# Performance work log

Hardware: AMD Instinct MI355X
Metric: run time of the kernel (lower is better)

The kernel has to match this reference:

```python
import jax, jax.numpy as jnp
import numpy as np


def _conv1x1(x, w, b):
    # x: (B,Ci,H,W), w: (Co,Ci) -> (B,Co,H,W)
    return jnp.einsum('bchw,oc->bohw', x, w) + b[None, :, None, None]


def _conv3x3(x, w, b):
    # x: (B,Ci,H,W), w: (Co,Ci,3,3), stride 1, padding 1 ('SAME')
    y = jax.lax.conv_general_dilated(
        x, w, window_strides=(1, 1), padding='SAME',
        dimension_numbers=('NCHW', 'OIHW', 'NCHW'))
    return y + b[None, :, None, None]


def setup_inputs() -> dict:
    key = jax.random.key(0)
    ks = jax.random.split(key, 10)
    N, B, Cc, Cf, H, W = 3, 8, 128, 256, 64, 64
    s = 0.05  # weight scale to keep attention logits well-conditioned
    return {
        'contexts': jax.random.normal(ks[0], (N, B, Cc, 2 * H, 2 * W), jnp.float32),
        'mainstream': jax.random.normal(ks[1], (B, Cf, H, W), jnp.float32),
        'Wc_w': jax.random.normal(ks[2], (Cc, Cc), jnp.float32) * s,
        'Wc_b': jax.random.normal(ks[3], (Cc,), jnp.float32) * s,
        'Wf_w': jax.random.normal(ks[4], (Cc, Cf), jnp.float32) * s,
        'Wf_b': jax.random.normal(ks[5], (Cc,), jnp.float32) * s,
        'Wk_w': jax.random.normal(ks[6], (Cc, Cf), jnp.float32) * s,
        'Wk_b': jax.random.normal(ks[7], (Cc,), jnp.float32) * s,
        'Wv_w': jax.random.normal(ks[8], (Cc, Cf, 3, 3), jnp.float32) * s,
        'Wv_b': jax.random.normal(ks[9], (Cc,), jnp.float32) * s,
    }


def reference(contexts, mainstream, Wc_w, Wc_b, Wf_w, Wf_b, Wk_w, Wk_b, Wv_w, Wv_b):
    N, B, Cc = contexts.shape[0], contexts.shape[1], contexts.shape[2]
    H, W = mainstream.shape[2], mainstream.shape[3]

    q = _conv1x1(mainstream, Wf_w, Wf_b)        # (B,Cc,H,W) queries
    mkey = _conv1x1(mainstream, Wk_w, Wk_b)     # (B,Cc,H,W) mainline keys
    vals = _conv3x3(mainstream, Wv_w, Wv_b)     # (B,Cc,H,W) mainline values
    ckeys = jax.vmap(lambda c: _conv1x1(c, Wc_w, Wc_b))(contexts)  # (N,B,Cc,2H,2W)

    # unfold 2x2 sub-pixel blocks: (.., 2H, 2W) -> (.., H, 2, W, 2)
    ckeys = ckeys.reshape(N, B, Cc, H, 2, W, 2)
    cfeat = contexts.reshape(N, B, Cc, H, 2, W, 2)

    # per-pixel cross-attention logits: context keys . query
    logits_ctx = jnp.einsum('nbchiwj,bchw->nbhiwj', ckeys, q)      # (N,B,H,2,W,2)
    # mainline key . query (same logit for all 4 sub-pixels)
    logit_main = jnp.einsum('bchw,bchw->bhw', mkey, q)[None, :, :, None, :, None]
    logits = jnp.concatenate(
        [logits_ctx, jnp.broadcast_to(logit_main, (1, B, H, 2, W, 2))], axis=0)

    attn = jax.nn.softmax(logits, axis=0)                          # (N+1,B,H,2,W,2)

    vfeat = jnp.broadcast_to(vals[None, :, :, :, None, :, None],
                             (1, B, Cc, H, 2, W, 2))
    feats = jnp.concatenate([cfeat, vfeat], axis=0)                # (N+1,B,Cc,H,2,W,2)

    out = jnp.einsum('nbhiwj,nbchiwj->bchiwj', attn, feats)        # (B,Cc,H,2,W,2)
    return out.reshape(B, Cc, 2 * H, 2 * W)
```

## Files before the change

### kernel.cpp

```cpp
#include <hip/hip_runtime.h>

#define NCTX 3
#define B 8
#define CC 128
#define CF 256
#define H 64
#define W 64
#define HW 4096
#define YX 16384

#define WS_QT    0
#define WS_VALS  4194304
#define WS_BIAS  8388608
#define WS_LM    8421376
#define WS_WALL  8454144
#define WS_MSP   8552960
#define WS_WB    13013504
#define WS_WALLO 13160960

typedef __attribute__((ext_vector_type(8))) short bf16x8;
typedef __attribute__((ext_vector_type(4))) float f32x4;
typedef __attribute__((ext_vector_type(8))) unsigned short u16x8;

__device__ __forceinline__ unsigned short f2b(float f) {
    union { float f; unsigned u; } c; c.f = f;
    unsigned u = c.u + 0x7FFFu + ((c.u >> 16) & 1u);
    return (unsigned short)(u >> 16);
}
__device__ __forceinline__ float b2f(unsigned short u) {
    union { unsigned u; float f; } c; c.u = ((unsigned)u) << 16;
    return c.f;
}

__global__ __launch_bounds__(256) void k0(
    const float* __restrict__ Wc_w, const float* __restrict__ Wc_b,
    const float* __restrict__ Wf_w, const float* __restrict__ Wf_b,
    const float* __restrict__ Wk_w, const float* __restrict__ Wk_b,
    const float* __restrict__ Wv, const float* __restrict__ ms,
    unsigned short* __restrict__ Wall, unsigned short* __restrict__ Wallo,
    float* __restrict__ bias448, unsigned short* __restrict__ Wb,
    unsigned short* __restrict__ msP) {
    __shared__ float Ls[32][65];
    int blk = blockIdx.x;
    int t = threadIdx.x;
    if (blk < 448) {
        int o = blk * 256 + t;
        int ci8 = o & 7;
        int idx = o >> 3;
        int row = idx % 448;
        int sc4 = idx / 448;
        int f = (sc4 >> 2) * 32 + (sc4 & 3) * 8 + ci8;
        float w;
        if (row < 128) {
            float s = 0.f;
            for (int o2 = 0; o2 < 128; ++o2) s += Wc_w[o2 * 128 + row] * Wf_w[o2 * 256 + f];
            w = s;
        } else if (row < 384) {
            int p = (row - 128) >> 1;
            w = (row & 1) ? Wk_w[p * 256 + f] : Wf_w[p * 256 + f];
        } else if (row == 384) {
            float s = 0.f;
            for (int o2 = 0; o2 < 128; ++o2) s += Wc_b[o2] * Wf_w[o2 * 256 + f];
            w = s;
        } else w = 0.f;
        unsigned short hi = f2b(w);
        Wall[o] = hi;
        Wallo[o] = f2b(w - b2f(hi));
        if (o < 448) {
            float bb;
            if (o < 128) {
                float s = 0.f;
                for (int o2 = 0; o2 < 128; ++o2) s += Wc_w[o2 * 128 + o] * Wf_b[o2];
                bb = s;
            } else if (o < 384) {
                int p = (o - 128) >> 1;
                bb = (o & 1) ? Wk_b[p] : Wf_b[p];
            } else if (o == 384) {
                float s = 0.f;
                for (int o2 = 0; o2 < 128; ++o2) s += Wc_b[o2] * Wf_b[o2];
                bb = s;
            } else if (o == 385) bb = -1.f;
            else bb = 0.f;
            bias448[o] = bb;
        }
    } else if (blk < 1600) {
        int o = (blk - 448) * 256 + t;
        int ci8 = o & 7;
        int co  = (o >> 3) & 127;
        int c4  = (o >> 10) & 3;
        int s   = (o >> 12) & 7;
        int khw = o >> 15;
        int ci  = s * 32 + c4 * 8 + ci8;
        int kh  = khw / 3, kw = khw - kh * 3;
        Wb[o] = f2b(Wv[((co * 256 + ci) * 3 + kh) * 3 + kw]);
    } else if (blk < 1860) {
        int i = (blk - 1600) * 256 + t;
        if (i < 66560) {
            size_t off;
            if (i < 33792) {
                int x = i % 66; int r = i / 66;
                int g = r & 31, rowi = (r >> 5) & 1, b = r >> 6;
                off = ((((size_t)b * 66 + rowi * 65) * 32) + g) * 66 + x;
            } else {
                int k = i - 33792;
                int xi = k & 1; int g = (k >> 1) & 31; int y1 = (k >> 6) & 63; int b = k >> 12;
                off = ((((size_t)b * 66 + (y1 + 1)) * 32) + g) * 66 + xi * 65;
            }
            *(u16x8*)&msP[off * 8] = (u16x8){0, 0, 0, 0, 0, 0, 0, 0};
        }
    } else {
        int local = blk - 1860;
        int s = local & 7;
        int h = (local >> 3) & 63;
        int b = local >> 9;
        const float* src = ms + ((size_t)b * 256 + s * 32) * HW + h * 64;
        for (int l = t; l < 2048; l += 256) {
            int ci = l >> 6, w = l & 63;
            Ls[ci][w] = src[ci * HW + w];
        }
        __syncthreads();
        int w = t & 63, gi = t >> 6;
        u16x8 vh;
#pragma unroll
        for (int j = 0; j < 8; ++j) vh[j] = f2b(Ls[gi * 8 + j][w]);
        size_t offH = ((((size_t)b * 66 + (h + 1)) * 32) + (s * 4 + gi)) * 66 + (w + 1);
        *(u16x8*)&msP[offH * 8] = vh;
    }
}

__global__ __launch_bounds__(512, 4) void kmm(
    const float* __restrict__ ms, const unsigned short* __restrict__ msP,
    const unsigned short* __restrict__ Wall, const unsigned short* __restrict__ Wallo,
    const float* __restrict__ bias448, const unsigned short* __restrict__ Wb,
    const float* __restrict__ Wv_b,
    float* __restrict__ qt, float* __restrict__ lm, float* __restrict__ vals) {
    __shared__ unsigned char smem[25856] __attribute__((aligned(16)));
    int t = threadIdx.x;
    int lane = t & 63, wid = t >> 6;
    int c4l = lane >> 4, lrow = lane & 15;
    int blk = blockIdx.x;

    if (blk < 512) {
        auto Bs = (unsigned short (*)[2][4][64][8])smem;
        float* biasS = (float*)(smem + 16384);
        float* lmAcc = (float*)(smem + 16384 + 1792);
        int wm = wid >> 1, wn = wid & 1;
        int b = blk >> 6, h = blk & 63;
        int xs = t & 63, g4 = t >> 6;
        int c4w = g4 >> 1, sub = g4 & 1;
        const float* msb = ms + ((size_t)b * 256 + g4 * 4) * HW + h * 64 + xs;
        for (int i = t; i < 448; i += 512) biasS[i] = bias448[i];
        if (t < 64) lmAcc[t] = 0.f;

        f32x4 acc[7][2];
#pragma unroll
        for (int mf = 0; mf < 7; ++mf)
#pragma unroll
            for (int nf = 0; nf < 2; ++nf) acc[mf][nf] = (f32x4){0.f, 0.f, 0.f, 0.f};

        const bf16x8* Whip = (const bf16x8*)Wall;
        const bf16x8* Wlop = (const bf16x8*)Wallo;

#define CVT_WRITE(bufv, F0, F1, F2, F3) do {                                    \
        unsigned short h0 = f2b(F0), h1 = f2b(F1), h2 = f2b(F2), h3 = f2b(F3);  \
        unsigned short q0 = f2b((F0) - b2f(h0)), q1 = f2b((F1) - b2f(h1));      \
        unsigned short q2 = f2b((F2) - b2f(h2)), q3 = f2b((F3) - b2f(h3));      \
        uint2 hw, lw;                                                           \
        hw.x = (unsigned)h0 | ((unsigned)h1 << 16);                             \
        hw.y = (unsigned)h2 | ((unsigned)h3 << 16);                             \
        lw.x = (unsigned)q0 | ((unsigned)q1 << 16);                             \
        lw.y = (unsigned)q2 | ((unsigned)q3 << 16);                             \
        *(uint2*)&Bs[bufv][0][c4w][xs][sub * 4] = hw;                           \
        *(uint2*)&Bs[bufv][1][c4w][xs][sub * 4] = lw;                           \
    } while (0)

        {
            float f0 = msb[0], f1 = msb[HW], f2 = msb[2 * HW], f3 = msb[3 * HW];
            CVT_WRITE(0, f0, f1, f2, f3);
        }
        __syncthreads();

        for (int s = 0; s < 8; ++s) {
            int cur = s & 1;
            float fn0, fn1, fn2, fn3;
            if (s < 7) {
                const float* p = msb + (size_t)(s + 1) * 32 * HW;
                fn0 = p[0]; fn1 = p[HW]; fn2 = p[2 * HW]; fn3 = p[3 * HW];
            }
            bf16x8 bh[2], bl[2];
#pragma unroll
            for (int nf = 0; nf < 2; ++nf) {
                int x = wn * 32 + nf * 16 + lrow;
                bh[nf] = *(const bf16x8*)&Bs[cur][0][c4l][x][0];
                bl[nf] = *(const bf16x8*)&Bs[cur][1][c4l][x][0];
            }
#pragma unroll
            for (int mf = 0; mf < 7; ++mf) {
                size_t widx = (size_t)(s * 4 + c4l) * 448 + wm * 112 + mf * 16 + lrow;
                bf16x8 ah = Whip[widx];
                bf16x8 al = Wlop[widx];
#pragma unroll
                for (int nf = 0; nf < 2; ++nf) {
                    acc[mf][nf] = __builtin_amdgcn_mfma_f32_16x16x32_bf16(ah, bh[nf], acc[mf][nf], 0, 0, 0);
                    acc[mf][nf] = __builtin_amdgcn_mfma_f32_16x16x32_bf16(ah, bl[nf], acc[mf][nf], 0, 0, 0);
                    acc[mf][nf] = __builtin_amdgcn_mfma_f32_16x16x32_bf16(al, bh[nf], acc[mf][nf], 0, 0, 0);
                }
            }
            if (s < 7) CVT_WRITE(cur ^ 1, fn0, fn1, fn2, fn3);
            __syncthreads();
        }
#undef CVT_WRITE

        int px0 = wn * 32;
        float lmp[2] = {0.f, 0.f};
#pragma unroll
        for (int mf = 0; mf < 7; ++mf) {
            int base = wm * 112 + mf * 16;
            int r0 = base + c4l * 4;
            if (base < 128) {
#pragma unroll
                for (int nf = 0; nf < 2; ++nf) {
                    int x = px0 + nf * 16 + lrow;
                    float* dst = qt + ((size_t)b * 128 + r0) * HW + h * 64 + x;
                    f32x4 v = acc[mf][nf];
#pragma unroll
                    for (int j = 0; j < 4; ++j)
                        dst[(size_t)j * HW] = v[j] + biasS[r0 + j];
                }
            } else {
                float b0 = biasS[r0], b1 = biasS[r0 + 1], b2 = biasS[r0 + 2], b3 = biasS[r0 + 3];
#pragma unroll
                for (int nf = 0; nf < 2; ++nf) {
                    f32x4 v = acc[mf][nf];
                    lmp[nf] += (v[0] + b0) * (v[1] + b1) + (v[2] + b2) * (v[3] + b3);
                }
            }
        }
        if (wm != 0) {
#pragma unroll
            for (int nf = 0; nf < 2; ++nf) {
                lmp[nf] += __shfl_xor(lmp[nf], 16);
                lmp[nf] += __shfl_xor(lmp[nf], 32);
            }
            if (c4l == 0) {
#pragma unroll
                for (int nf = 0; nf < 2; ++nf)
                    atomicAdd(&lmAcc[px0 + nf * 16 + lrow], lmp[nf]);
            }
        }
        __syncthreads();
        if (t < 64) lm[b * HW + h * 64 + t] = lmAcc[t];
    } else {
        auto Bs = (unsigned short (*)[6336])smem;
        float* biasS = (float*)(smem + 25344);
        int local = blk - 512;
        int b = local >> 6;
        int hl = local & 63;
        int h = ((hl & 7) << 3) | (hl >> 3);
        int wm = wid >> 1, wn = wid & 1;
        if (t < 128) biasS[t] = Wv_b[t];

        f32x4 acc[2][2];
#pragma unroll
        for (int mf = 0; mf < 2; ++mf)
#pragma unroll
            for (int nf = 0; nf < 2; ++nf) acc[mf][nf] = (f32x4){0.f, 0.f, 0.f, 0.f};

        const bf16x8* Wbp = (const bf16x8*)Wb;

#define STAGE2(bufv, sv) do {                                                       \
        for (int iter = 0; iter < 2; ++iter) {                                      \
            int q0 = iter * 512 + (wid << 6);                                       \
            int q = q0 + lane;                                                      \
            if (q < 792) {                                                          \
                int rc = q / 66; int x = q - rc * 66;                               \
                int r = rc >> 2, c4 = rc & 3;                                       \
                int y = h + r;                               \
                const unsigned short* gp = msP +                                    \
                    (((((size_t)b * 66 + y) * 32) + ((sv) * 4 + c4)) * 66 + x) * 8; \
                unsigned short* lp = &Bs[bufv][q0 * 8];                             \
                __builtin_amdgcn_global_load_lds(                                   \
                    (const __attribute__((address_space(1))) void*)gp,              \
                    (__attribute__((address_space(3))) void*)lp, 16, 0, 0);         \
            }                                                                       \
        }                                                                           \
    } while (0)

        STAGE2(0, 0);
        __syncthreads();

        for (int s = 0; s < 8; ++s) {
            int cur = s & 1;
            if (s < 7) STAGE2(cur ^ 1, s + 1);
#pragma unroll
            for (int khw = 0; khw < 9; ++khw) {
                int kh = khw / 3, kw = khw - 3 * (khw / 3);
                bf16x8 a[2];
#pragma unroll
                for (int mf = 0; mf < 2; ++mf)
                    a[mf] = Wbp[((khw * 8 + s) * 4 + c4l) * 128 + wm * 32 + mf * 16 + lrow];
                bf16x8 bf[2];
#pragma unroll
                for (int nf = 0; nf < 2; ++nf) {
                    int chunk = (kh * 4 + c4l) * 66 + wn * 32 + nf * 16 + lrow + kw;
                    bf[nf] = *(const bf16x8*)&Bs[cur][chunk * 8];
                }
#pragma unroll
                for (int mf = 0; mf < 2; ++mf)
#pragma unroll
                    for (int nf = 0; nf < 2; ++nf)
                        acc[mf][nf] = __builtin_amdgcn_mfma_f32_16x16x32_bf16(
                            a[mf], bf[nf], acc[mf][nf], 0, 0, 0);
            }
            __syncthreads();
        }
#undef STAGE2

#pragma unroll
        for (int mf = 0; mf < 2; ++mf) {
            int co0 = wm * 32 + mf * 16 + c4l * 4;
#pragma unroll
            for (int nf = 0; nf < 2; ++nf) {
                int x = wn * 32 + nf * 16 + lrow;
                float* dst = vals + (((size_t)b * 128 + co0) * HW) + h * 64 + x;
                f32x4 v = acc[mf][nf];
#pragma unroll
                for (int j = 0; j < 4; ++j)
                    dst[(size_t)j * HW] = v[j] + biasS[co0 + j];
            }
        }
    }
}

__global__ __launch_bounds__(256, 2) void k3(
    const float* __restrict__ ctx, const float* __restrict__ qt,
    const float* __restrict__ vals, const float* __restrict__ lm,
    float* __restrict__ out) {
    __shared__ float part[4][3][64];
    __shared__ float attnS[4][64];
    int t = threadIdx.x;
    int lane = t & 63, wv = t >> 6;
    int xg = t & 15, cq = t >> 4;
    int blk = blockIdx.x;
    int b = blk >> 8, y = (blk >> 1) & 127, xh = blk & 1;
    int h = y >> 1;
    int x0 = xh * 64 + xg * 4;
    int p0 = xh * 32 + xg * 2;

    float2 qv[8], vv[8];
    const float* qbase = qt + ((size_t)b * 128 + cq * 8) * HW + h * 64 + p0;
    const float* vbase = vals + ((size_t)b * 128 + cq * 8) * HW + h * 64 + p0;
#pragma unroll
    for (int j = 0; j < 8; ++j) {
        qv[j] = *(const float2*)&qbase[(size_t)j * HW];
        vv[j] = *(const float2*)&vbase[(size_t)j * HW];
    }
    float4 cx[3][8];
#pragma unroll
    for (int n = 0; n < 3; ++n) {
        const float* cb = ctx + ((size_t)(n * 8 + b) * 128 + cq * 8) * YX + (size_t)y * 128 + x0;
#pragma unroll
        for (int j = 0; j < 8; ++j) cx[n][j] = *(const float4*)&cb[(size_t)j * YX];
    }
    float lp[3][4];
#pragma unroll
    for (int n = 0; n < 3; ++n) {
#pragma unroll
        for (int xl = 0; xl < 4; ++xl) lp[n][xl] = 0.f;
#pragma unroll
        for (int j = 0; j < 8; ++j) {
            lp[n][0] += cx[n][j].x * qv[j].x;
            lp[n][1] += cx[n][j].y * qv[j].x;
            lp[n][2] += cx[n][j].z * qv[j].y;
            lp[n][3] += cx[n][j].w * qv[j].y;
        }
    }
#pragma unroll
    for (int n = 0; n < 3; ++n)
#pragma unroll
        for (int xl = 0; xl < 4; ++xl) {
            float v = lp[n][xl];
            v += __shfl_xor(v, 16);
            v += __shfl_xor(v, 32);
            lp[n][xl] = v;
        }
    if (lane < 16) {
#pragma unroll
        for (int n = 0; n < 3; ++n)
#pragma unroll
            for (int xl = 0; xl < 4; ++xl)
                part[wv][n][lane * 4 + xl] = lp[n][xl];
    }
    __syncthreads();
    if (t < 64) {
        float l0 = part[0][0][t] + part[1][0][t] + part[2][0][t] + part[3][0][t];
        float l1 = part[0][1][t] + part[1][1][t] + part[2][1][t] + part[3][1][t];
        float l2 = part[0][2][t] + part[1][2][t] + part[2][2][t] + part[3][2][t];
        float l3 = lm[(size_t)b * HW + h * 64 + xh * 32 + (t >> 1)];
        float m = fmaxf(fmaxf(l0, l1), fmaxf(l2, l3));
        float e0 = __expf(l0 - m), e1 = __expf(l1 - m), e2 = __expf(l2 - m), e3 = __expf(l3 - m);
        float inv = 1.f / (e0 + e1 + e2 + e3);
        attnS[0][t] = e0 * inv; attnS[1][t] = e1 * inv;
        attnS[2][t] = e2 * inv; attnS[3][t] = e3 * inv;
    }
    __syncthreads();
    float a0[4], a1[4], a2[4], a3[4];
#pragma unroll
    for (int xl = 0; xl < 4; ++xl) {
        a0[xl] = attnS[0][xg * 4 + xl];
        a1[xl] = attnS[1][xg * 4 + xl];
        a2[xl] = attnS[2][xg * 4 + xl];
        a3[xl] = attnS[3][xg * 4 + xl];
    }
    float* obase = out + ((size_t)b * 128 + cq * 8) * YX + (size_t)y * 128 + x0;
#pragma unroll
    for (int j = 0; j < 8; ++j) {
        float4 o;
        o.x = a3[0] * vv[j].x + a0[0] * cx[0][j].x + a1[0] * cx[1][j].x + a2[0] * cx[2][j].x;
        o.y = a3[1] * vv[j].x + a0[1] * cx[0][j].y + a1[1] * cx[1][j].y + a2[1] * cx[2][j].y;
        o.z = a3[2] * vv[j].y + a0[2] * cx[0][j].z + a1[2] * cx[1][j].z + a2[2] * cx[2][j].z;
        o.w = a3[3] * vv[j].y + a0[3] * cx[0][j].w + a1[3] * cx[1][j].w + a2[3] * cx[2][j].w;
        *(float4*)&obase[(size_t)j * YX] = o;
    }
}

extern "C" void kernel_launch(void* const* d_in, const int* in_sizes, int n_in,
                              void* d_out, int out_size, void* d_ws, size_t ws_size,
                              hipStream_t stream) {
    const float* ctx  = (const float*)d_in[0];
    const float* ms   = (const float*)d_in[1];
    const float* Wc_w = (const float*)d_in[2];
    const float* Wc_b = (const float*)d_in[3];
    const float* Wf_w = (const float*)d_in[4];
    const float* Wf_b = (const float*)d_in[5];
    const float* Wk_w = (const float*)d_in[6];
    const float* Wk_b = (const float*)d_in[7];
    const float* Wv_w = (const float*)d_in[8];
    const float* Wv_b = (const float*)d_in[9];
    float* out = (float*)d_out;
    float* ws = (float*)d_ws;
    float* qt      = ws + WS_QT;
    float* vals    = ws + WS_VALS;
    float* bias448 = ws + WS_BIAS;
    float* lmp     = ws + WS_LM;
    unsigned short* Wallp  = (unsigned short*)(ws + WS_WALL);
    unsigned short* Wallop = (unsigned short*)(ws + WS_WALLO);
    unsigned short* msPp   = (unsigned short*)(ws + WS_MSP);
    unsigned short* Wbp    = (unsigned short*)(ws + WS_WB);

    hipLaunchKernelGGL(k0, dim3(5956), dim3(256), 0, stream, Wc_w, Wc_b, Wf_w, Wf_b,
                       Wk_w, Wk_b, Wv_w, ms, Wallp, Wallop, bias448, Wbp, msPp);
    hipLaunchKernelGGL(kmm, dim3(1024), dim3(512), 0, stream, ms, msPp, Wallp, Wallop,
                       bias448, Wbp, Wv_b, qt, lmp, vals);
    hipLaunchKernelGGL(k3, dim3(2048), dim3(256), 0, stream, ctx, qt, vals, lmp, out);
}
```

Before: 146.3 us.

## Store q and vals intermediates as bf16, remap k3 blocks, raise occupancy

The matmul kernel now writes the query projection and 3x3 value intermediates in bf16 rather than fp32, halving their write and reread traffic between kmm and k3. k3 unpacks bf16 pairs, defers the value load until after the softmax, restructures the logit reduction per context to cut register pressure, raises its launch bound to 4 blocks per SM, and swizzles the block index across batches. Precision of the intermediates drops, which adds rounding error to logits and outputs.

```diff
diff --git a/kernel.cpp b/kernel.cpp
--- a/kernel.cpp
+++ b/kernel.cpp
@@ -133,7 +133,8 @@
     const unsigned short* __restrict__ Wall, const unsigned short* __restrict__ Wallo,
     const float* __restrict__ bias448, const unsigned short* __restrict__ Wb,
     const float* __restrict__ Wv_b,
-    float* __restrict__ qt, float* __restrict__ lm, float* __restrict__ vals) {
+    unsigned short* __restrict__ qtB, float* __restrict__ lm,
+    unsigned short* __restrict__ valsB) {
     __shared__ unsigned char smem[25856] __attribute__((aligned(16)));
     int t = threadIdx.x;
     int lane = t & 63, wid = t >> 6;
@@ -221,11 +222,11 @@
 #pragma unroll
                 for (int nf = 0; nf < 2; ++nf) {
                     int x = px0 + nf * 16 + lrow;
-                    float* dst = qt + ((size_t)b * 128 + r0) * HW + h * 64 + x;
+                    unsigned short* dst = qtB + ((size_t)b * 128 + r0) * HW + h * 64 + x;
                     f32x4 v = acc[mf][nf];
 #pragma unroll
                     for (int j = 0; j < 4; ++j)
-                        dst[(size_t)j * HW] = v[j] + biasS[r0 + j];
+                        dst[(size_t)j * HW] = f2b(v[j] + biasS[r0 + j]);
                 }
             } else {
                 float b0 = biasS[r0], b1 = biasS[r0 + 1], b2 = biasS[r0 + 2], b3 = biasS[r0 + 3];
@@ -322,38 +323,39 @@
 #pragma unroll
             for (int nf = 0; nf < 2; ++nf) {
                 int x = wn * 32 + nf * 16 + lrow;
-                float* dst = vals + (((size_t)b * 128 + co0) * HW) + h * 64 + x;
+                unsigned short* dst = valsB + (((size_t)b * 128 + co0) * HW) + h * 64 + x;
                 f32x4 v = acc[mf][nf];
 #pragma unroll
                 for (int j = 0; j < 4; ++j)
-                    dst[(size_t)j * HW] = v[j] + biasS[co0 + j];
-            }
-        }
-    }
-}
-
-__global__ __launch_bounds__(256, 2) void k3(
-    const float* __restrict__ ctx, const float* __restrict__ qt,
-    const float* __restrict__ vals, const float* __restrict__ lm,
+                    dst[(size_t)j * HW] = f2b(v[j] + biasS[co0 + j]);
+            }
+        }
+    }
+}
+
+__global__ __launch_bounds__(256, 4) void k3(
+    const float* __restrict__ ctx, const unsigned short* __restrict__ qtB,
+    const unsigned short* __restrict__ valsB, const float* __restrict__ lm,
     float* __restrict__ out) {
     __shared__ float part[4][3][64];
     __shared__ float attnS[4][64];
     int t = threadIdx.x;
     int lane = t & 63, wv = t >> 6;
     int xg = t & 15, cq = t >> 4;
-    int blk = blockIdx.x;
+    int blk0 = blockIdx.x;
+    int blk = (blk0 & 7) * 256 + (blk0 >> 3);
     int b = blk >> 8, y = (blk >> 1) & 127, xh = blk & 1;
     int h = y >> 1;
     int x0 = xh * 64 + xg * 4;
     int p0 = xh * 32 + xg * 2;
 
-    float2 qv[8], vv[8];
-    const float* qbase = qt + ((size_t)b * 128 + cq * 8) * HW + h * 64 + p0;
-    const float* vbase = vals + ((size_t)b * 128 + cq * 8) * HW + h * 64 + p0;
+    const unsigned short* qb = qtB + ((size_t)b * 128 + cq * 8) * HW + h * 64 + p0;
+    float qvx[8], qvy[8];
 #pragma unroll
     for (int j = 0; j < 8; ++j) {
-        qv[j] = *(const float2*)&qbase[(size_t)j * HW];
-        vv[j] = *(const float2*)&vbase[(size_t)j * HW];
+        unsigned v = *(const unsigned*)&qb[(size_t)j * HW];
+        qvx[j] = b2f((unsigned short)(v & 0xffffu));
+        qvy[j] = b2f((unsigned short)(v >> 16));
     }
     float4 cx[3][8];
 #pragma unroll
@@ -362,34 +364,28 @@
 #pragma unroll
         for (int j = 0; j < 8; ++j) cx[n][j] = *(const float4*)&cb[(size_t)j * YX];
     }
-    float lp[3][4];
 #pragma unroll
     for (int n = 0; n < 3; ++n) {
-#pragma unroll
-        for (int xl = 0; xl < 4; ++xl) lp[n][xl] = 0.f;
+        float lp[4] = {0.f, 0.f, 0.f, 0.f};
 #pragma unroll
         for (int j = 0; j < 8; ++j) {
-            lp[n][0] += cx[n][j].x * qv[j].x;
-            lp[n][1] += cx[n][j].y * qv[j].x;
-            lp[n][2] += cx[n][j].z * qv[j].y;
-            lp[n][3] += cx[n][j].w * qv[j].y;
-        }
-    }
-#pragma unroll
-    for (int n = 0; n < 3; ++n)
+            lp[0] += cx[n][j].x * qvx[j];
+            lp[1] += cx[n][j].y * qvx[j];
+            lp[2] += cx[n][j].z * qvy[j];
+            lp[3] += cx[n][j].w * qvy[j];
+        }
 #pragma unroll
         for (int xl = 0; xl < 4; ++xl) {
-            float v = lp[n][xl];
+            float v = lp[xl];
             v += __shfl_xor(v, 16);
             v += __shfl_xor(v, 32);
-            lp[n][xl] = v;
-        }
-    if (lane < 16) {
-#pragma unroll
-        for (int n = 0; n < 3; ++n)
+            lp[xl] = v;
+        }
+        if (lane < 16) {
 #pragma unroll
             for (int xl = 0; xl < 4; ++xl)
-                part[wv][n][lane * 4 + xl] = lp[n][xl];
+                part[wv][n][lane * 4 + xl] = lp[xl];
+        }
     }
     __syncthreads();
     if (t < 64) {
@@ -404,6 +400,10 @@
         attnS[2][t] = e2 * inv; attnS[3][t] = e3 * inv;
     }
     __syncthreads();
+    const unsigned short* vb = valsB + ((size_t)b * 128 + cq * 8) * HW + h * 64 + p0;
+    unsigned vvp[8];
+#pragma unroll
+    for (int j = 0; j < 8; ++j) vvp[j] = *(const unsigned*)&vb[(size_t)j * HW];
     float a0[4], a1[4], a2[4], a3[4];
 #pragma unroll
     for (int xl = 0; xl < 4; ++xl) {
@@ -415,11 +415,13 @@
     float* obase = out + ((size_t)b * 128 + cq * 8) * YX + (size_t)y * 128 + x0;
 #pragma unroll
     for (int j = 0; j < 8; ++j) {
+        float vx = b2f((unsigned short)(vvp[j] & 0xffffu));
+        float vy = b2f((unsigned short)(vvp[j] >> 16));
         float4 o;
-        o.x = a3[0] * vv[j].x + a0[0] * cx[0][j].x + a1[0] * cx[1][j].x + a2[0] * cx[2][j].x;
-        o.y = a3[1] * vv[j].x + a0[1] * cx[0][j].y + a1[1] * cx[1][j].y + a2[1] * cx[2][j].y;
-        o.z = a3[2] * vv[j].y + a0[2] * cx[0][j].z + a1[2] * cx[1][j].z + a2[2] * cx[2][j].z;
-        o.w = a3[3] * vv[j].y + a0[3] * cx[0][j].w + a1[3] * cx[1][j].w + a2[3] * cx[2][j].w;
+        o.x = a3[0] * vx + a0[0] * cx[0][j].x + a1[0] * cx[1][j].x + a2[0] * cx[2][j].x;
+        o.y = a3[1] * vx + a0[1] * cx[0][j].y + a1[1] * cx[1][j].y + a2[1] * cx[2][j].y;
+        o.z = a3[2] * vy + a0[2] * cx[0][j].z + a1[2] * cx[1][j].z + a2[2] * cx[2][j].z;
+        o.w = a3[3] * vy + a0[3] * cx[0][j].w + a1[3] * cx[1][j].w + a2[3] * cx[2][j].w;
         *(float4*)&obase[(size_t)j * YX] = o;
     }
 }
@@ -439,10 +441,10 @@
     const float* Wv_b = (const float*)d_in[9];
     float* out = (float*)d_out;
     float* ws = (float*)d_ws;
-    float* qt      = ws + WS_QT;
-    float* vals    = ws + WS_VALS;
     float* bias448 = ws + WS_BIAS;
     float* lmp     = ws + WS_LM;
+    unsigned short* qtBp   = (unsigned short*)(ws + WS_QT);
+    unsigned short* valsBp = (unsigned short*)(ws + WS_VALS);
     unsigned short* Wallp  = (unsigned short*)(ws + WS_WALL);
     unsigned short* Wallop = (unsigned short*)(ws + WS_WALLO);
     unsigned short* msPp   = (unsigned short*)(ws + WS_MSP);
@@ -451,6 +453,6 @@
     hipLaunchKernelGGL(k0, dim3(5956), dim3(256), 0, stream, Wc_w, Wc_b, Wf_w, Wf_b,
                        Wk_w, Wk_b, Wv_w, ms, Wallp, Wallop, bias448, Wbp, msPp);
     hipLaunchKernelGGL(kmm, dim3(1024), dim3(512), 0, stream, ms, msPp, Wallp, Wallop,
-                       bias448, Wbp, Wv_b, qt, lmp, vals);
-    hipLaunchKernelGGL(k3, dim3(2048), dim3(256), 0, stream, ctx, qt, vals, lmp, out);
-}
+                       bias448, Wbp, Wv_b, qtBp, lmp, valsBp);
+    hipLaunchKernelGGL(k3, dim3(2048), dim3(256), 0, stream, ctx, qtBp, valsBp, lmp, out);
+}
```

Measured after the change: 159.2 us. 8.8% more time.
